# Kernel optimization log

Hardware: AMD Instinct MI355X
Metric: run time of the kernel (lower is better)

## Reference

```python
import jax, jax.numpy as jnp
import numpy as np

B = 4096          # number of graphs in the batch
D = 256           # ORB node feature dim (out_dim)
AVG_NODES = 128   # average nodes per graph
N_TOTAL = B * AVG_NODES


def setup_inputs() -> dict:
    key = jax.random.key(0)
    # Ragged per-graph node counts that sum exactly to N_TOTAL.
    rng = np.random.default_rng(0)
    counts = rng.multinomial(N_TOTAL, np.full(B, 1.0 / B))  # ~128 each, all >0 w.h.p.
    n_nodes = jnp.asarray(counts, dtype=jnp.int32)
    node_feats = jax.random.normal(key, (N_TOTAL, D), dtype=jnp.float32)
    return {"node_feats": node_feats, "n_nodes": n_nodes}


def reference(node_feats, n_nodes):
    # Fused segment-mean: one pass over nodes instead of B small kernels.
    n_total = node_feats.shape[0]
    b = n_nodes.shape[0]
    # segment id for every node: [0,0,...,1,1,...,B-1,...]
    seg_ids = jnp.repeat(jnp.arange(b, dtype=jnp.int32), n_nodes,
                         total_repeat_length=n_total)
    sums = jax.ops.segment_sum(node_feats, seg_ids, num_segments=b)  # (B, D)
    graph_feats = sums / n_nodes[:, None].astype(node_feats.dtype)
    return graph_feats
```

## Files before the change

kernel.cpp:

```cpp
#include <hip/hip_runtime.h>


#define B_GRAPHS 4096
#define DIM 256
#define SCAN_THREADS 256
#define PER_THREAD (B_GRAPHS / SCAN_THREADS)

__global__ __launch_bounds__(SCAN_THREADS) void scan_offsets(
    const int* __restrict__ n_nodes, int* __restrict__ offsets) {
  __shared__ int tsum[SCAN_THREADS];
  const int t = threadIdx.x;

  int vals[PER_THREAD];
  int s = 0;
#pragma unroll
  for (int i = 0; i < PER_THREAD; ++i) {
    vals[i] = n_nodes[t * PER_THREAD + i];
    s += vals[i];
  }
  tsum[t] = s;
  __syncthreads();

#pragma unroll
  for (int d = 1; d < SCAN_THREADS; d <<= 1) {
    int add = (t >= d) ? tsum[t - d] : 0;
    __syncthreads();
    tsum[t] += add;
    __syncthreads();
  }

  int excl = (t == 0) ? 0 : tsum[t - 1];
#pragma unroll
  for (int i = 0; i < PER_THREAD; ++i) {
    offsets[t * PER_THREAD + i] = excl;
    excl += vals[i];
  }
}

__global__ __launch_bounds__(256) void seg_mean(
    const float* __restrict__ feats, const int* __restrict__ n_nodes,
    const int* __restrict__ offsets, float* __restrict__ out) {
  const int tid = threadIdx.x;
  const int lane = tid & 63;
  const int g = blockIdx.x * 4 + (tid >> 6);

  const int start = offsets[g];
  const int n = n_nodes[g];

  const float4* __restrict__ src =
      reinterpret_cast<const float4*>(feats) + (size_t)start * 64 + lane;

  float4 a0 = make_float4(0.f, 0.f, 0.f, 0.f);
  float4 a1 = a0, a2 = a0, a3 = a0;

  int r = 0;
  for (; r + 4 <= n; r += 4) {
    float4 v0 = src[(size_t)(r + 0) * 64];
    float4 v1 = src[(size_t)(r + 1) * 64];
    float4 v2 = src[(size_t)(r + 2) * 64];
    float4 v3 = src[(size_t)(r + 3) * 64];
    a0.x += v0.x; a0.y += v0.y; a0.z += v0.z; a0.w += v0.w;
    a1.x += v1.x; a1.y += v1.y; a1.z += v1.z; a1.w += v1.w;
    a2.x += v2.x; a2.y += v2.y; a2.z += v2.z; a2.w += v2.w;
    a3.x += v3.x; a3.y += v3.y; a3.z += v3.z; a3.w += v3.w;
  }
  for (; r < n; ++r) {
    float4 v = src[(size_t)r * 64];
    a0.x += v.x; a0.y += v.y; a0.z += v.z; a0.w += v.w;
  }

  float4 acc;
  acc.x = (a0.x + a1.x) + (a2.x + a3.x);
  acc.y = (a0.y + a1.y) + (a2.y + a3.y);
  acc.z = (a0.z + a1.z) + (a2.z + a3.z);
  acc.w = (a0.w + a1.w) + (a2.w + a3.w);

  const float inv = 1.0f / (float)n;
  acc.x *= inv; acc.y *= inv; acc.z *= inv; acc.w *= inv;

  reinterpret_cast<float4*>(out)[(size_t)g * 64 + lane] = acc;
}

extern "C" void kernel_launch(void* const* d_in, const int* in_sizes, int n_in,
                              void* d_out, int out_size, void* d_ws, size_t ws_size,
                              hipStream_t stream) {
  const float* node_feats = (const float*)d_in[0];
  const int* n_nodes = (const int*)d_in[1];
  float* out = (float*)d_out;
  int* offsets = (int*)d_ws;

  scan_offsets<<<1, SCAN_THREADS, 0, stream>>>(n_nodes, offsets);
  seg_mean<<<B_GRAPHS / 4, 256, 0, stream>>>(node_feats, n_nodes, offsets, out);
}
```

Baseline: 684.9 us.

## Fuse offset scan into segment-mean kernel via per-block prefix reduction

Removes the separate single-block scan kernel. Each block now computes its own starting offset by reducing n_nodes over all preceding graphs in shared memory, then sums its graphs' rows. The inner accumulation loop is also unrolled to 8 independent float4 accumulators. This saves one launch and the serialized scan, but every block rereads a prefix of n_nodes, which is redundant O(B^2) work of small size, and the wider unroll raises register use.

```diff
diff --git a/kernel.cpp b/kernel.cpp
--- a/kernel.cpp
+++ b/kernel.cpp
@@ -1,84 +1,67 @@
 #include <hip/hip_runtime.h>
 
 
-#define B_GRAPHS 4096
-#define DIM 256
-#define SCAN_THREADS 256
-#define PER_THREAD (B_GRAPHS / SCAN_THREADS)
+#define BLOCK 256
+#define GPB 4
 
-__global__ __launch_bounds__(SCAN_THREADS) void scan_offsets(
-    const int* __restrict__ n_nodes, int* __restrict__ offsets) {
-  __shared__ int tsum[SCAN_THREADS];
+typedef float f4 __attribute__((ext_vector_type(4)));
+
+__global__ __launch_bounds__(BLOCK) void seg_mean_fused(
+    const float* __restrict__ feats,
+    const int* __restrict__ n_nodes,
+    float* __restrict__ out) {
+  __shared__ int red[BLOCK];
+  __shared__ int offs[GPB];
+
   const int t = threadIdx.x;
+  const int g0 = blockIdx.x * GPB;
 
-  int vals[PER_THREAD];
   int s = 0;
+  for (int i = t; i < g0; i += BLOCK) s += n_nodes[i];
+  red[t] = s;
+  __syncthreads();
 #pragma unroll
-  for (int i = 0; i < PER_THREAD; ++i) {
-    vals[i] = n_nodes[t * PER_THREAD + i];
-    s += vals[i];
+  for (int d = BLOCK / 2; d > 0; d >>= 1) {
+    if (t < d) red[t] += red[t + d];
+    __syncthreads();
   }
-  tsum[t] = s;
+  if (t == 0) {
+    int o = red[0];
+#pragma unroll
+    for (int j = 0; j < GPB; ++j) {
+      offs[j] = o;
+      o += n_nodes[g0 + j];
+    }
+  }
   __syncthreads();
 
+  const int wave = t >> 6;
+  const int lane = t & 63;
+  const int g = g0 + wave;
+  const int n = n_nodes[g];
+  const int start = offs[wave];
+
+  const f4* __restrict__ src =
+      reinterpret_cast<const f4*>(feats) + (size_t)start * 64 + lane;
+
+  f4 acc[8];
 #pragma unroll
-  for (int d = 1; d < SCAN_THREADS; d <<= 1) {
-    int add = (t >= d) ? tsum[t - d] : 0;
-    __syncthreads();
-    tsum[t] += add;
-    __syncthreads();
-  }
-
-  int excl = (t == 0) ? 0 : tsum[t - 1];
-#pragma unroll
-  for (int i = 0; i < PER_THREAD; ++i) {
-    offsets[t * PER_THREAD + i] = excl;
-    excl += vals[i];
-  }
-}
-
-__global__ __launch_bounds__(256) void seg_mean(
-    const float* __restrict__ feats, const int* __restrict__ n_nodes,
-    const int* __restrict__ offsets, float* __restrict__ out) {
-  const int tid = threadIdx.x;
-  const int lane = tid & 63;
-  const int g = blockIdx.x * 4 + (tid >> 6);
-
-  const int start = offsets[g];
-  const int n = n_nodes[g];
-
-  const float4* __restrict__ src =
-      reinterpret_cast<const float4*>(feats) + (size_t)start * 64 + lane;
-
-  float4 a0 = make_float4(0.f, 0.f, 0.f, 0.f);
-  float4 a1 = a0, a2 = a0, a3 = a0;
+  for (int i = 0; i < 8; ++i) acc[i] = (f4)0.0f;
 
   int r = 0;
-  for (; r + 4 <= n; r += 4) {
-    float4 v0 = src[(size_t)(r + 0) * 64];
-    float4 v1 = src[(size_t)(r + 1) * 64];
-    float4 v2 = src[(size_t)(r + 2) * 64];
-    float4 v3 = src[(size_t)(r + 3) * 64];
-    a0.x += v0.x; a0.y += v0.y; a0.z += v0.z; a0.w += v0.w;
-    a1.x += v1.x; a1.y += v1.y; a1.z += v1.z; a1.w += v1.w;
-    a2.x += v2.x; a2.y += v2.y; a2.z += v2.z; a2.w += v2.w;
-    a3.x += v3.x; a3.y += v3.y; a3.z += v3.z; a3.w += v3.w;
+  for (; r + 8 <= n; r += 8) {
+#pragma unroll
+    for (int i = 0; i < 8; ++i) {
+      acc[i] += src[(size_t)(r + i) * 64];
+    }
   }
-  for (; r < n; ++r) {
-    float4 v = src[(size_t)r * 64];
-    a0.x += v.x; a0.y += v.y; a0.z += v.z; a0.w += v.w;
-  }
+  for (; r < n; ++r) acc[0] += src[(size_t)r * 64];
 
-  float4 acc;
-  acc.x = (a0.x + a1.x) + (a2.x + a3.x);
-  acc.y = (a0.y + a1.y) + (a2.y + a3.y);
-  acc.z = (a0.z + a1.z) + (a2.z + a3.z);
-  acc.w = (a0.w + a1.w) + (a2.w + a3.w);
+  f4 total = ((acc[0] + acc[1]) + (acc[2] + acc[3])) +
+             ((acc[4] + acc[5]) + (acc[6] + acc[7]));
+  total *= (1.0f / (float)n);
 
-  const float inv = 1.0f / (float)n;
-  acc.x *= inv; acc.y *= inv; acc.z *= inv; acc.w *= inv;
-
-  reinterpret_cast<float4*>(out)[(size_t)g * 64 + lane] = acc;
+  reinterpret_cast<f4*>(out)[(size_t)g * 64 + lane] = total;
 }
 
 extern "C" void kernel_launch(void* const* d_in, const int* in_sizes, int n_in,
@@ -87,8 +70,7 @@
   const float* node_feats = (const float*)d_in[0];
   const int* n_nodes = (const int*)d_in[1];
   float* out = (float*)d_out;
-  int* offsets = (int*)d_ws;
 
-  scan_offsets<<<1, SCAN_THREADS, 0, stream>>>(n_nodes, offsets);
-  seg_mean<<<B_GRAPHS / 4, 256, 0, stream>>>(node_feats, n_nodes, offsets, out);
+  const int b = in_sizes[1];
+  seg_mean_fused<<<b / GPB, BLOCK, 0, stream>>>(node_feats, n_nodes, out);
 }
```

Result: no change. 682.5 us (-0.3%).
